# Kernel optimization log

Measured on AMD Instinct MI355X. Metric: run time of the kernel, lower is better.

The kernel has to match this reference:

```python
import jax, jax.numpy as jnp
import numpy as np

NTYPES = 2
B, N, MNEI = 4, 512, 100
M = MNEI * NTYPES          # neighbor slots = maxNeighborNum * ntypes
EMB_LAST = 100             # embedding net sizes [25, 50, 100]
FIT_H = 240
M2 = 16
RMIN, RMAX = 0.5, 6.0


def setup_inputs():
    key = jax.random.key(0)
    ks = jax.random.split(key, 24)
    r = jax.random.uniform(ks[0], (B, N, M), minval=0.6, maxval=7.0)
    v = jax.random.normal(ks[1], (B, N, M, 3))
    v = v / jnp.linalg.norm(v, axis=-1, keepdims=True)
    keep = jax.random.uniform(ks[2], (B, N, M)) < 0.7
    ImageDR = jnp.concatenate([r[..., None], r[..., None] * v], axis=-1)
    ImageDR = jnp.where(keep[..., None], ImageDR, 0.0).astype(jnp.float32)
    Imagetype_map = jax.random.randint(ks[3], (N,), 0, NTYPES)
    list_neigh = jax.random.randint(ks[4], (B, N, M), 0, N + 1)
    type_map = jnp.arange(NTYPES)
    davg = (0.01 * jax.random.normal(ks[5], (NTYPES, M, 4))).astype(jnp.float32)
    dstd = (1.0 + 0.1 * jax.random.uniform(ks[6], (NTYPES, M, 4))).astype(jnp.float32)

    def w(k, shape, fan):
        return (jax.random.normal(k, shape) / np.sqrt(fan)).astype(jnp.float32)

    def b(k, shape):
        return (0.1 * jax.random.normal(k, shape)).astype(jnp.float32)

    emb_W0 = w(ks[7], (NTYPES, NTYPES, 1, 25), 1)
    emb_b0 = b(ks[8], (NTYPES, NTYPES, 25))
    emb_W1 = w(ks[9], (NTYPES, NTYPES, 25, 50), 25)
    emb_b1 = b(ks[10], (NTYPES, NTYPES, 50))
    emb_W2 = w(ks[11], (NTYPES, NTYPES, 50, 100), 50)
    emb_b2 = b(ks[12], (NTYPES, NTYPES, 100))
    fin = M2 * EMB_LAST
    fit_W0 = w(ks[13], (NTYPES, fin, FIT_H), fin)
    fit_b0 = b(ks[14], (NTYPES, FIT_H))
    fit_W1 = w(ks[15], (NTYPES, FIT_H, FIT_H), FIT_H)
    fit_b1 = b(ks[16], (NTYPES, FIT_H))
    fit_W2 = w(ks[17], (NTYPES, FIT_H, FIT_H), FIT_H)
    fit_b2 = b(ks[18], (NTYPES, FIT_H))
    fit_W3 = w(ks[19], (NTYPES, FIT_H, 1), FIT_H)
    fit_b3 = b(ks[20], (NTYPES, 1))
    energy_shift = jnp.array([-3.37, -5.21], dtype=jnp.float32)
    return dict(list_neigh=list_neigh, Imagetype_map=Imagetype_map, type_map=type_map,
                ImageDR=ImageDR, nghost=0, davg=davg, dstd=dstd,
                emb_W0=emb_W0, emb_b0=emb_b0, emb_W1=emb_W1, emb_b1=emb_b1,
                emb_W2=emb_W2, emb_b2=emb_b2,
                fit_W0=fit_W0, fit_b0=fit_b0, fit_W1=fit_W1, fit_b1=fit_b1,
                fit_W2=fit_W2, fit_b2=fit_b2, fit_W3=fit_W3, fit_b3=fit_b3,
                energy_shift=energy_shift)


def _emb(s, W0, b0, W1, b1, W2, b2):
    # DeepPot-SE embedding net with doubling resnet connections
    h = jnp.tanh(s @ W0 + b0)                                   # [..., 25]
    h = jnp.tanh(h @ W1 + b1) + jnp.concatenate([h, h], -1)     # [..., 50]
    return jnp.tanh(h @ W2 + b2) + jnp.concatenate([h, h], -1)  # [..., 100]


def _fit(d, W0, b0, W1, b1, W2, b2, W3, b3):
    h = jnp.tanh(d @ W0 + b0)
    h = h + jnp.tanh(h @ W1 + b1)
    h = h + jnp.tanh(h @ W2 + b2)
    return h @ W3 + b3


def _forward(ImageDR, davg, dstd,
             emb_W0, emb_b0, emb_W1, emb_b1, emb_W2, emb_b2,
             fit_W0, fit_b0, fit_W1, fit_b1, fit_W2, fit_b2, fit_W3, fit_b3,
             energy_shift, Imagetype_map):
    Bsz, Nat, Mtot, _ = ImageDR.shape
    m = Mtot // NTYPES
    R = ImageDR[..., 0]
    Rsafe = jnp.where(R > 1e-5, R, 1.0)
    # smooth switching function s(r): 1/r below Rmin, polynomial taper to Rmax
    u = (R - RMIN) / (RMAX - RMIN)
    mid = (u ** 3 * (-6.0 * u * u + 15.0 * u - 10.0) + 1.0) / Rsafe
    S = jnp.where((R > 0) & (R < RMIN), 1.0 / Rsafe,
                  jnp.where((R > RMIN) & (R < RMAX), mid, 0.0))
    msk = (jnp.abs(R) > 1e-5)[..., None]
    Ri = jnp.concatenate([S[..., None],
                          jnp.where(msk, (S / Rsafe)[..., None] * ImageDR[..., 1:4], 0.0)],
                         axis=-1)                                    # [B,N,M,4] = (s, s*x/r, s*y/r, s*z/r)
    # per-center-type normalization (irregular gather of stats)
    Rn = (Ri - davg[Imagetype_map][None]) / dstd[Imagetype_map][None]
    tmask = [(Imagetype_map == i).astype(Rn.dtype)[None, :, None, None] for i in range(NTYPES)]
    xyz = jnp.zeros((Bsz, Nat, 4, EMB_LAST), Rn.dtype)
    for j in range(NTYPES):                                          # neighbor-type slice
        sl = Rn[:, :, j * m:(j + 1) * m, :]                          # [B,N,m,4]
        s = sl[..., 0:1]
        G = jnp.zeros(sl.shape[:3] + (EMB_LAST,), sl.dtype)
        for i in range(NTYPES):                                      # center type -> pair net (i, j)
            G = G + tmask[i] * _emb(s, emb_W0[i, j], emb_b0[i, j],
                                    emb_W1[i, j], emb_b1[i, j], emb_W2[i, j], emb_b2[i, j])
        xyz = xyz + jnp.einsum('bnmk,bnmc->bnkc', sl, G)
    xyz = xyz / (m * NTYPES)
    # descriptor D = (Ri^T G)^T (Ri^T G)[:, :M2], flattened -> [B,N,EMB_LAST*M2]
    D = jnp.einsum('bnkc,bnkd->bncd', xyz, xyz[..., :M2]).reshape(Bsz, Nat, -1)
    Ei = jnp.zeros((Bsz, Nat), D.dtype)
    for i in range(NTYPES):
        e = _fit(D, fit_W0[i], fit_b0[i], fit_W1[i], fit_b1[i],
                 fit_W2[i], fit_b2[i], fit_W3[i], fit_b3[i])[..., 0] + energy_shift[i]
        Ei = Ei + tmask[i][:, :, 0, 0] * e
    Etot = jnp.sum(Ei, axis=1)
    return Etot, Ei


def reference(list_neigh, Imagetype_map, type_map, ImageDR, nghost, davg, dstd,
              emb_W0, emb_b0, emb_W1, emb_b1, emb_W2, emb_b2,
              fit_W0, fit_b0, fit_W1, fit_b1, fit_W2, fit_b2, fit_W3, fit_b3,
              energy_shift):
    return _forward(ImageDR, davg, dstd,
                    emb_W0, emb_b0, emb_W1, emb_b1, emb_W2, emb_b2,
                    fit_W0, fit_b0, fit_W1, fit_b1, fit_W2, fit_b2, fit_W3, fit_b3,
                    energy_shift, Imagetype_map)
```

## Files before the change

kernel.cpp:

```cpp
#include <hip/hip_runtime.h>
#include <math.h>

#define NT 2
#define BSZ 4
#define NAT 512
#define NATOMS 2048
#define NNEI 200
#define EMB 100
#define FITH 240
#define DDIM 1600
#define TBK 1024

#define BIAS_F  16
#define W3C_F   (BIAS_F + 3 * 512)
#define USH_BYTE 8320
#define TBL_U   0
#define W0T_U   409600
#define W1T_U   (W0T_U + 819200)
#define W2T_U   (W1T_U + 262144)
#define D_U     (W2T_U + 262144)
#define H0_U    (D_U + 3276800)
#define H1_U    (H0_U + 1048576)
#define USH_END (H1_U + 1048576)
#define WS_NEED ((size_t)USH_BYTE + (size_t)USH_END * 2)

typedef short s8v __attribute__((ext_vector_type(8)));
typedef float f4v __attribute__((ext_vector_type(4)));

__device__ __forceinline__ float ftanh(float x) {
    float ax = fabsf(x);
    float e = __expf(2.0f * ax);
    float t = 1.0f - __fdividef(2.0f, e + 1.0f);
    return (x < 0.0f) ? -t : t;
}
__device__ __forceinline__ unsigned short f2bf(float f) {
    unsigned u = __float_as_uint(f);
    u += 0x7FFFu + ((u >> 16) & 1u);
    return (unsigned short)(u >> 16);
}
__device__ __forceinline__ float bf2f(unsigned short s) {
    return __uint_as_float(((unsigned)s) << 16);
}
__device__ __forceinline__ float calc_S(float R) {
    float Rsafe = (R > 1e-5f) ? R : 1.0f;
    float u = (R - 0.5f) * (1.0f / 5.5f);
    float uu = u * u;
    float mid = (u * uu * (-6.0f * uu + 15.0f * u - 10.0f) + 1.0f) / Rsafe;
    float S = 0.0f;
    if (R > 0.0f && R < 0.5f)      S = 1.0f / Rsafe;
    else if (R > 0.5f && R < 6.0f) S = mid;
    return S;
}

#define N_W0 819200
#define N_W1 262144
#define N_W2 262144
#define N_B  1536
#define N_W3 512
#define N_EI 2048
__global__ void wtrans_kernel(const float* __restrict__ fW0, const float* __restrict__ fW1,
                              const float* __restrict__ fW2,
                              const float* __restrict__ fb0, const float* __restrict__ fb1,
                              const float* __restrict__ fb2,
                              const float* __restrict__ fW3, const float* __restrict__ fb3,
                              const float* __restrict__ eshift, const int* __restrict__ itype,
                              float* __restrict__ ws, float* __restrict__ out) {
    unsigned short* u0 = (unsigned short*)((char*)ws + USH_BYTE);
    int id = blockIdx.x * 256 + threadIdx.x;
    if (id < N_W0) {
        int n = id / 1600, k = id - n * 1600;
        float v = 0.0f;
        if (n < 240)                  v = fW0[(size_t)k * 240 + n];
        else if (n >= 256 && n < 496) v = fW0[(size_t)(1600 + k) * 240 + (n - 256)];
        u0[W0T_U + id] = f2bf(v);
        return;
    }
    id -= N_W0;
    if (id < N_W1) {
        int n = id / 512, k = id - n * 512;
        float v = 0.0f;
        if (n < 240 && k < 240)       v = fW1[(size_t)k * 240 + n];
        else if (n >= 256 && n < 496 && k >= 256 && k < 496)
                                      v = fW1[(size_t)(240 + (k - 256)) * 240 + (n - 256)];
        u0[W1T_U + id] = f2bf(v);
        return;
    }
    id -= N_W1;
    if (id < N_W2) {
        int n = id / 512, k = id - n * 512;
        float v = 0.0f;
        if (n < 240 && k < 240)       v = fW2[(size_t)k * 240 + n];
        else if (n >= 256 && n < 496 && k >= 256 && k < 496)
                                      v = fW2[(size_t)(240 + (k - 256)) * 240 + (n - 256)];
        u0[W2T_U + id] = f2bf(v);
        return;
    }
    id -= N_W2;
    if (id < N_B) {
        int l = id / 512, n = id - l * 512;
        const float* fb = (l == 0) ? fb0 : (l == 1) ? fb1 : fb2;
        float v = 0.0f;
        if (n < 240)                  v = fb[n];
        else if (n >= 256 && n < 496) v = fb[240 + (n - 256)];
        ws[BIAS_F + l * 512 + n] = v;
        return;
    }
    id -= N_B;
    if (id < N_W3) {
        int n = id;
        float v = 0.0f;
        if (n < 240)                  v = fW3[n];
        else if (n >= 256 && n < 496) v = fW3[240 + (n - 256)];
        ws[W3C_F + n] = v;
        return;
    }
    id -= N_W3;
    if (id < N_EI) {
        int t = itype[id & (NAT - 1)];
        out[4 + id] = fb3[t] + eshift[t];
    }
}

__global__ void __launch_bounds__(256) table_kernel(
    const float* __restrict__ davg, const float* __restrict__ dstd,
    const float* __restrict__ eW0, const float* __restrict__ eb0,
    const float* __restrict__ eW1, const float* __restrict__ eb1,
    const float* __restrict__ eW2, const float* __restrict__ eb2,
    float* __restrict__ ws)
{
    __shared__ float los[100], his[100];
    __shared__ float rng[2];
    __shared__ float h0s[8][25];
    __shared__ float h1s[8][50];
    const int bx = blockIdx.x;
    const int nid = bx >> 7;
    const int kb  = (bx & 127) * 8;
    const int t = nid >> 1, j = nid & 1;
    const int tid = threadIdx.x;

    if (tid < 100) {
        int m = j * 100 + tid;
        float av = davg[(t * NNEI + m) * 4];
        float sd = dstd[(t * NNEI + m) * 4];
        float inv = __fdividef(1.0f, sd);
        float a = (0.0f - av) * inv;
        float b = (2.0f - av) * inv;
        los[tid] = fminf(a, b);
        his[tid] = fmaxf(a, b);
    }
    __syncthreads();
    if (tid == 0) {
        float lo = los[0], hi = his[0];
        for (int i = 1; i < 100; ++i) { lo = fminf(lo, los[i]); hi = fmaxf(hi, his[i]); }
        rng[0] = lo; rng[1] = hi - lo;
        if (kb == 0) {
            ws[nid * 2] = lo;
            ws[nid * 2 + 1] = (float)(TBK - 1) / (hi - lo);
        }
    }
    __syncthreads();
    const float smin = rng[0], span = rng[1];
    const float* W0 = eW0 + nid * 25;
    const float* B0 = eb0 + nid * 25;
    if (tid < 200) {
        int q = tid / 25, a = tid % 25;
        float s = smin + span * ((float)(kb + q) * (1.0f / (TBK - 1)));
        h0s[q][a] = ftanh(fmaf(s, W0[a], B0[a]));
    }
    __syncthreads();
    const float* W1 = eW1 + nid * 1250;
    const float* B1 = eb1 + nid * 50;
    for (int idx = tid; idx < 400; idx += 256) {
        int q = idx / 50, cc = idx % 50;
        float acc = B1[cc];
#pragma unroll
        for (int a = 0; a < 25; ++a) acc = fmaf(h0s[q][a], W1[a * 50 + cc], acc);
        h1s[q][cc] = ftanh(acc) + h0s[q][(cc < 25) ? cc : cc - 25];
    }
    __syncthreads();
    const float* W2 = eW2 + nid * 5000;
    const float* B2 = eb2 + nid * 100;
    unsigned short* tblu = (unsigned short*)((char*)ws + USH_BYTE) + TBL_U;
    for (int idx = tid; idx < 800; idx += 256) {
        int q = idx / 100, c = idx % 100;
        float acc = B2[c];
#pragma unroll
        for (int a = 0; a < 50; ++a) acc = fmaf(h1s[q][a], W2[a * 100 + c], acc);
        float g = ftanh(acc) + h1s[q][(c < 50) ? c : c - 50];
        tblu[(size_t)(nid * TBK + kb + q) * 100 + c] = f2bf(g);
    }
}

__global__ void __launch_bounds__(128) embed_kernel(
    const int* __restrict__ itype, const float* __restrict__ imagedr,
    const float* __restrict__ davg, const float* __restrict__ dstd,
    float* __restrict__ ws)
{
    __shared__ __align__(16) float4 srn[NNEI];
    __shared__ float sx[NNEI];
    __shared__ float part[2][400];
    const int atom = blockIdx.x;
    const int n = atom & (NAT - 1);
    const int tid = threadIdx.x;
    const int t = itype[n];
    unsigned short* u0 = (unsigned short*)((char*)ws + USH_BYTE);

    const float sm0 = ws[(t * 2 + 0) * 2], sc0 = ws[(t * 2 + 0) * 2 + 1];
    const float sm1 = ws[(t * 2 + 1) * 2], sc1 = ws[(t * 2 + 1) * 2 + 1];

    for (int m = tid; m < NNEI; m += 128) {
        float4 dr = ((const float4*)imagedr)[(size_t)atom * NNEI + m];
        float R = dr.x;
        float S = calc_S(R);
        float Rsafe = (R > 1e-5f) ? R : 1.0f;
        float sr = (fabsf(R) > 1e-5f) ? (S / Rsafe) : 0.0f;
        float4 av = ((const float4*)davg)[t * NNEI + m];
        float4 sd = ((const float4*)dstd)[t * NNEI + m];
        float4 rv;
        rv.x = (S         - av.x) / sd.x;
        rv.y = (sr * dr.y - av.y) / sd.y;
        rv.z = (sr * dr.z - av.z) / sd.z;
        rv.w = (sr * dr.w - av.w) / sd.w;
        srn[m] = rv;
        float smin = (m >= 100) ? sm1 : sm0;
        float scal = (m >= 100) ? sc1 : sc0;
        sx[m] = fminf(fmaxf((rv.x - smin) * scal, 0.0f), (float)(TBK - 2) + 0.9999f);
    }
    __syncthreads();

    const int w = tid >> 6, lane = tid & 63;
    const unsigned short* T = u0 + TBL_U + (size_t)(t * 2 + w) * TBK * EMB;
    const bool hi = (lane < 36);
    float xA0 = 0, xA1 = 0, xA2 = 0, xA3 = 0;
    float xB0 = 0, xB1 = 0, xB2 = 0, xB3 = 0;
#pragma unroll 2
    for (int mi = 0; mi < 100; ++mi) {
        int m = w * 100 + mi;
        float4 rv = srn[m];
        float x = sx[m];
        int i = (int)x;
        float f = x - (float)i;
        const unsigned short* Tr = T + (size_t)i * EMB;
        float g0 = bf2f(Tr[lane]);
        float g1 = bf2f(Tr[EMB + lane]);
        float g = fmaf(f, g1 - g0, g0);
        xA0 = fmaf(rv.x, g, xA0); xA1 = fmaf(rv.y, g, xA1);
        xA2 = fmaf(rv.z, g, xA2); xA3 = fmaf(rv.w, g, xA3);
        if (hi) {
            float h0v = bf2f(Tr[64 + lane]);
            float h1v = bf2f(Tr[EMB + 64 + lane]);
            float g2 = fmaf(f, h1v - h0v, h0v);
            xB0 = fmaf(rv.x, g2, xB0); xB1 = fmaf(rv.y, g2, xB1);
            xB2 = fmaf(rv.z, g2, xB2); xB3 = fmaf(rv.w, g2, xB3);
        }
    }
    part[w][0 * 100 + lane] = xA0; part[w][1 * 100 + lane] = xA1;
    part[w][2 * 100 + lane] = xA2; part[w][3 * 100 + lane] = xA3;
    if (hi) {
        part[w][0 * 100 + 64 + lane] = xB0; part[w][1 * 100 + 64 + lane] = xB1;
        part[w][2 * 100 + 64 + lane] = xB2; part[w][3 * 100 + 64 + lane] = xB3;
    }
    __syncthreads();
    const float inv = 1.0f / 200.0f;
    for (int idx = tid; idx < 400; idx += 128)
        part[0][idx] = (part[0][idx] + part[1][idx]) * inv;
    __syncthreads();
    unsigned short* Drow = u0 + D_U + (size_t)atom * DDIM;
    const float* xt = part[0];
    for (int idx = tid; idx < DDIM; idx += 128) {
        int c = idx >> 4, d = idx & 15;
        float s = xt[c] * xt[d] + xt[100 + c] * xt[100 + d]
                + xt[200 + c] * xt[200 + d] + xt[300 + c] * xt[300 + d];
        Drow[idx] = f2bf(s);
    }
}

__global__ void __launch_bounds__(64) gemm16_kernel(
    const unsigned short* __restrict__ A, int lda,
    const unsigned short* __restrict__ BT, int ldb,
    const float* __restrict__ bias,
    const unsigned short* __restrict__ Res,
    unsigned short* __restrict__ Out, int ldo,
    const float* __restrict__ w3c, const int* __restrict__ itype,
    float* __restrict__ out,
    int ksteps, int diag, int mode)
{
    const int lane = threadIdx.x;
    const int bx = blockIdx.x;
    const int by = blockIdx.y;
    const int m0 = by * 16, n0 = bx * 32;
    const int k0 = (diag && bx >= 8) ? 256 : 0;
    const int mr = lane & 15;
    const int q  = lane >> 4;
    const unsigned short* Ap  = A  + (size_t)(m0 + mr) * lda + k0 + q * 8;
    const unsigned short* B0p = BT + (size_t)(n0 + mr) * ldb + k0 + q * 8;
    const unsigned short* B1p = B0p + (size_t)16 * ldb;

    f4v acc0 = {0.0f, 0.0f, 0.0f, 0.0f};
    f4v acc1 = {0.0f, 0.0f, 0.0f, 0.0f};
#pragma unroll 2
    for (int kt = 0; kt < ksteps; ++kt) {
        s8v av = *(const s8v*)(Ap  + kt * 32);
        s8v b0 = *(const s8v*)(B0p + kt * 32);
        s8v b1 = *(const s8v*)(B1p + kt * 32);
        acc0 = __builtin_amdgcn_mfma_f32_16x16x32_bf16(av, b0, acc0, 0, 0, 0);
        acc1 = __builtin_amdgcn_mfma_f32_16x16x32_bf16(av, b1, acc1, 0, 0, 0);
    }

    const int g0 = n0 + mr, g1 = n0 + 16 + mr;
    const float bv0 = bias[g0], bv1 = bias[g1];
    if (mode < 2) {
#pragma unroll
        for (int r = 0; r < 4; ++r) {
            int row = m0 + q * 4 + r;
            size_t i0 = (size_t)row * ldo + g0;
            size_t i1 = (size_t)row * ldo + g1;
            float v0 = ftanh(acc0[r] + bv0);
            float v1 = ftanh(acc1[r] + bv1);
            if (mode == 1) { v0 += bf2f(Res[i0]); v1 += bf2f(Res[i1]); }
            Out[i0] = f2bf(v0); Out[i1] = f2bf(v1);
        }
    } else {
        const int seg = (bx >= 8);
        const float w30 = w3c[g0], w31 = w3c[g1];
#pragma unroll
        for (int r = 0; r < 4; ++r) {
            int row = m0 + q * 4 + r;
            size_t i0 = (size_t)row * ldo + g0;
            size_t i1 = (size_t)row * ldo + g1;
            float v0 = bf2f(Res[i0]) + ftanh(acc0[r] + bv0);
            float v1 = bf2f(Res[i1]) + ftanh(acc1[r] + bv1);
            float p = v0 * w30 + v1 * w31;
            p += __shfl_xor(p, 1, 16);
            p += __shfl_xor(p, 2, 16);
            p += __shfl_xor(p, 4, 16);
            p += __shfl_xor(p, 8, 16);
            if (mr == 0 && itype[row & (NAT - 1)] == seg)
                atomicAdd(&out[4 + row], p);
        }
    }
}

__global__ void etot_kernel(float* __restrict__ out) {
    const int b = blockIdx.x;
    float s = 0.0f;
    for (int n = threadIdx.x; n < NAT; n += 256) s += out[4 + b * NAT + n];
#pragma unroll
    for (int off = 32; off > 0; off >>= 1) s += __shfl_down(s, off, 64);
    __shared__ float rr[4];
    if ((threadIdx.x & 63) == 0) rr[threadIdx.x >> 6] = s;
    __syncthreads();
    if (threadIdx.x == 0) out[b] = rr[0] + rr[1] + rr[2] + rr[3];
}

__global__ void dp_atom_kernel(
    const int* __restrict__ itype, const float* __restrict__ imagedr,
    const float* __restrict__ davg, const float* __restrict__ dstd,
    const float* __restrict__ eW0, const float* __restrict__ eb0,
    const float* __restrict__ eW1, const float* __restrict__ eb1,
    const float* __restrict__ eW2, const float* __restrict__ eb2,
    const float* __restrict__ fW0, const float* __restrict__ fb0,
    const float* __restrict__ fW1, const float* __restrict__ fb1,
    const float* __restrict__ fW2, const float* __restrict__ fb2,
    const float* __restrict__ fW3, const float* __restrict__ fb3,
    const float* __restrict__ eshift, float* __restrict__ out)
{
    __shared__ __align__(16) float4 rn4[NNEI];
    __shared__ __align__(16) float  xyz[4 * EMB];
    __shared__ __align__(16) float  h0s[100 * 25];
    __shared__ __align__(16) float  smem[100 * 52];
    const int atom = blockIdx.x;
    const int n = atom & (NAT - 1);
    const int tid = threadIdx.x;
    const int t = itype[n];
    for (int m = tid; m < NNEI; m += 256) {
        float4 dr = ((const float4*)imagedr)[(size_t)atom * NNEI + m];
        float R = dr.x;
        float S = calc_S(R);
        float Rsafe = (R > 1e-5f) ? R : 1.0f;
        float sr = (fabsf(R) > 1e-5f) ? (S / Rsafe) : 0.0f;
        float4 av = ((const float4*)davg)[t * NNEI + m];
        float4 sd = ((const float4*)dstd)[t * NNEI + m];
        float4 rv;
        rv.x = (S - av.x) / sd.x; rv.y = (sr * dr.y - av.y) / sd.y;
        rv.z = (sr * dr.z - av.z) / sd.z; rv.w = (sr * dr.w - av.w) / sd.w;
        rn4[m] = rv;
    }
    const int c = tid & 127; const int mh = tid >> 7;
    float xp0 = 0, xp1 = 0, xp2 = 0, xp3 = 0;
    for (int j = 0; j < NT; ++j) {
        const int wb = t * NT + j;
        const float* W0 = eW0 + wb * 25; const float* B0 = eb0 + wb * 25;
        const float* W1 = eW1 + wb * 1250; const float* B1 = eb1 + wb * 50;
        const float* W2 = eW2 + wb * 5000; const float* B2 = eb2 + wb * 100;
        __syncthreads();
        for (int idx = tid; idx < 2500; idx += 256) {
            int m = idx / 25, a = idx - m * 25;
            h0s[idx] = ftanh(fmaf(rn4[j * 100 + m].x, W0[a], B0[a]));
        }
        __syncthreads();
        for (int idx = tid; idx < 5000; idx += 256) {
            int m = idx / 50, cc = idx - m * 50;
            const float* h0m = h0s + m * 25;
            float acc = B1[cc];
#pragma unroll
            for (int a = 0; a < 25; ++a) acc = fmaf(h0m[a], W1[a * 50 + cc], acc);
            smem[m * 52 + cc] = ftanh(acc) + h0m[(cc < 25) ? cc : cc - 25];
        }
        for (int idx = tid; idx < 200; idx += 256)
            smem[(idx >> 1) * 52 + 50 + (idx & 1)] = 0.0f;
        __syncthreads();
        if (c < EMB) {
            float w2c[52];
#pragma unroll
            for (int a = 0; a < 50; ++a) w2c[a] = W2[a * EMB + c];
            w2c[50] = 0; w2c[51] = 0;
            const float bc = B2[c];
            const int sk = (c < 50) ? c : c - 50;
            for (int i = 0; i < 50; ++i) {
                int m = mh * 50 + i;
                const float* h1m = smem + m * 52;
                float acc = bc;
#pragma unroll
                for (int q = 0; q < 13; ++q) {
                    float4 hv = ((const float4*)h1m)[q];
                    acc = fmaf(hv.x, w2c[4 * q], acc); acc = fmaf(hv.y, w2c[4 * q + 1], acc);
                    acc = fmaf(hv.z, w2c[4 * q + 2], acc); acc = fmaf(hv.w, w2c[4 * q + 3], acc);
                }
                float g = ftanh(acc) + h1m[sk];
                float4 rm = rn4[j * 100 + m];
                xp0 = fmaf(rm.x, g, xp0); xp1 = fmaf(rm.y, g, xp1);
                xp2 = fmaf(rm.z, g, xp2); xp3 = fmaf(rm.w, g, xp3);
            }
        }
    }
    __syncthreads();
    const float inv = 1.0f / 200.0f;
    if (mh == 0 && c < EMB) {
        xyz[c] = xp0 * inv; xyz[EMB + c] = xp1 * inv;
        xyz[2 * EMB + c] = xp2 * inv; xyz[3 * EMB + c] = xp3 * inv;
    }
    __syncthreads();
    if (mh == 1 && c < EMB) {
        xyz[c] += xp0 * inv; xyz[EMB + c] += xp1 * inv;
        xyz[2 * EMB + c] += xp2 * inv; xyz[3 * EMB + c] += xp3 * inv;
    }
    __syncthreads();
    float* Dld = smem;
    for (int idx = tid; idx < DDIM; idx += 256) {
        int cc = idx >> 4, d = idx & 15;
        Dld[idx] = xyz[cc] * xyz[d] + xyz[EMB + cc] * xyz[EMB + d]
                 + xyz[2 * EMB + cc] * xyz[2 * EMB + d] + xyz[3 * EMB + cc] * xyz[3 * EMB + d];
    }
    __syncthreads();
    float* hA = smem + DDIM; float* hB = hA + FITH; float* h2 = hB + FITH; float* red = h2 + FITH;
    if (tid < FITH) {
        const float* W = fW0 + (size_t)t * DDIM * FITH;
        float acc = fb0[t * FITH + tid];
        for (int f = 0; f < DDIM; f += 4) {
            float4 dv = *(const float4*)(Dld + f);
            acc = fmaf(dv.x, W[f * FITH + tid], acc); acc = fmaf(dv.y, W[(f + 1) * FITH + tid], acc);
            acc = fmaf(dv.z, W[(f + 2) * FITH + tid], acc); acc = fmaf(dv.w, W[(f + 3) * FITH + tid], acc);
        }
        hA[tid] = ftanh(acc);
    }
    __syncthreads();
    if (tid < FITH) {
        const float* W = fW1 + t * FITH * FITH;
        float acc = fb1[t * FITH + tid];
        for (int f = 0; f < FITH; f += 4) {
            float4 hv = *(const float4*)(hA + f);
            acc = fmaf(hv.x, W[f * FITH + tid], acc); acc = fmaf(hv.y, W[(f + 1) * FITH + tid], acc);
            acc = fmaf(hv.z, W[(f + 2) * FITH + tid], acc); acc = fmaf(hv.w, W[(f + 3) * FITH + tid], acc);
        }
        hB[tid] = hA[tid] + ftanh(acc);
    }
    __syncthreads();
    if (tid < FITH) {
        const float* W = fW2 + t * FITH * FITH;
        float acc = fb2[t * FITH + tid];
        for (int f = 0; f < FITH; f += 4) {
            float4 hv = *(const float4*)(hB + f);
            acc = fmaf(hv.x, W[f * FITH + tid], acc); acc = fmaf(hv.y, W[(f + 1) * FITH + tid], acc);
            acc = fmaf(hv.z, W[(f + 2) * FITH + tid], acc); acc = fmaf(hv.w, W[(f + 3) * FITH + tid], acc);
        }
        h2[tid] = hB[tid] + ftanh(acc);
    }
    __syncthreads();
    float p = (tid < FITH) ? h2[tid] * fW3[t * FITH + tid] : 0.0f;
#pragma unroll
    for (int off = 32; off > 0; off >>= 1) p += __shfl_down(p, off, 64);
    if ((tid & 63) == 0) red[tid >> 6] = p;
    __syncthreads();
    if (tid == 0) out[4 + atom] = red[0] + red[1] + red[2] + red[3] + fb3[t] + eshift[t];
}

extern "C" void kernel_launch(void* const* d_in, const int* in_sizes, int n_in,
                              void* d_out, int out_size, void* d_ws, size_t ws_size,
                              hipStream_t stream) {
    const int*   itype   = (const int*)  d_in[1];
    const float* imagedr = (const float*)d_in[3];
    const float* davg    = (const float*)d_in[5];
    const float* dstd    = (const float*)d_in[6];
    const float* eW0     = (const float*)d_in[7];
    const float* eb0     = (const float*)d_in[8];
    const float* eW1     = (const float*)d_in[9];
    const float* eb1     = (const float*)d_in[10];
    const float* eW2     = (const float*)d_in[11];
    const float* eb2     = (const float*)d_in[12];
    const float* fW0     = (const float*)d_in[13];
    const float* fb0     = (const float*)d_in[14];
    const float* fW1     = (const float*)d_in[15];
    const float* fb1     = (const float*)d_in[16];
    const float* fW2     = (const float*)d_in[17];
    const float* fb2     = (const float*)d_in[18];
    const float* fW3     = (const float*)d_in[19];
    const float* fb3     = (const float*)d_in[20];
    const float* eshift  = (const float*)d_in[21];
    float* out = (float*)d_out;
    float* ws  = (float*)d_ws;

    if (ws_size >= WS_NEED) {
        unsigned short* u0 = (unsigned short*)((char*)ws + USH_BYTE);
        const int n_ids = N_W0 + N_W1 + N_W2 + N_B + N_W3 + N_EI;
        wtrans_kernel<<<(n_ids + 255) / 256, 256, 0, stream>>>(
            fW0, fW1, fW2, fb0, fb1, fb2, fW3, fb3, eshift, itype, ws, out);
        table_kernel<<<512, 256, 0, stream>>>(davg, dstd, eW0, eb0, eW1, eb1, eW2, eb2, ws);
        embed_kernel<<<NATOMS, 128, 0, stream>>>(itype, imagedr, davg, dstd, ws);
        gemm16_kernel<<<dim3(16, 128), 64, 0, stream>>>(
            u0 + D_U, DDIM, u0 + W0T_U, DDIM, ws + BIAS_F,
            nullptr, u0 + H0_U, 512, nullptr, nullptr, nullptr, 50, 0, 0);
        gemm16_kernel<<<dim3(16, 128), 64, 0, stream>>>(
            u0 + H0_U, 512, u0 + W1T_U, 512, ws + BIAS_F + 512,
            u0 + H0_U, u0 + H1_U, 512, nullptr, nullptr, nullptr, 8, 1, 0 + 1);
        gemm16_kernel<<<dim3(16, 128), 64, 0, stream>>>(
            u0 + H1_U, 512, u0 + W2T_U, 512, ws + BIAS_F + 1024,
            u0 + H1_U, nullptr, 512, ws + W3C_F, itype, out, 8, 1, 2);
        etot_kernel<<<BSZ, 256, 0, stream>>>(out);
    } else {
        dp_atom_kernel<<<NATOMS, 256, 0, stream>>>(itype, imagedr, davg, dstd,
            eW0, eb0, eW1, eb1, eW2, eb2,
            fW0, fb0, fW1, fb1, fW2, fb2, fW3, fb3, eshift, out);
        etot_kernel<<<BSZ, 256, 0, stream>>>(out);
    }
}
```

Before: 202.9 us.

## Widen fitting GEMM tiles to 64 columns and split-K the first layer

Replaces the generic 16x32-tile GEMM with two specialized kernels that compute 16x64 output tiles, so each A fragment load feeds four MFMAs instead of two. The first fitting layer now uses two waves that each take half of the K=1600 range, with the partial sums combined through shared memory before the bias+tanh epilogue. The residual layers hardcode K=256 per segment and fully unroll. The embed loop unroll factor also goes from 2 to 4. These trade more registers per wave and fewer blocks for better operand reuse and more parallel depth on the long K loop.

```diff
diff --git a/kernel.cpp b/kernel.cpp
--- a/kernel.cpp
+++ b/kernel.cpp
@@ -233,7 +233,7 @@
     const bool hi = (lane < 36);
     float xA0 = 0, xA1 = 0, xA2 = 0, xA3 = 0;
     float xB0 = 0, xB1 = 0, xB2 = 0, xB3 = 0;
-#pragma unroll 2
+#pragma unroll 4
     for (int mi = 0; mi < 100; ++mi) {
         int m = w * 100 + mi;
         float4 rv = srn[m];
@@ -275,62 +275,113 @@
     }
 }
 
-__global__ void __launch_bounds__(64) gemm16_kernel(
-    const unsigned short* __restrict__ A, int lda,
-    const unsigned short* __restrict__ BT, int ldb,
+__global__ void __launch_bounds__(128) gemm0_kernel(
+    const unsigned short* __restrict__ A,
+    const unsigned short* __restrict__ BT,
     const float* __restrict__ bias,
-    const unsigned short* __restrict__ Res,
-    unsigned short* __restrict__ Out, int ldo,
+    unsigned short* __restrict__ Out)
+{
+    __shared__ float lred[64][17];
+    const int tid = threadIdx.x;
+    const int w = tid >> 6, lane = tid & 63;
+    const int mr = lane & 15, q = lane >> 4;
+    const int n0 = blockIdx.x * 64;
+    const int m0 = blockIdx.y * 16;
+    const unsigned short* Ap = A  + (size_t)(m0 + mr) * DDIM + w * 800 + q * 8;
+    const unsigned short* Bp = BT + (size_t)(n0 + mr) * DDIM + w * 800 + q * 8;
+
+    f4v a0 = {0,0,0,0}, a1 = {0,0,0,0}, a2 = {0,0,0,0}, a3 = {0,0,0,0};
+#pragma unroll 5
+    for (int kt = 0; kt < 25; ++kt) {
+        s8v av = *(const s8v*)(Ap + kt * 32);
+        s8v b0 = *(const s8v*)(Bp + kt * 32);
+        s8v b1 = *(const s8v*)(Bp + 16 * DDIM + kt * 32);
+        s8v b2 = *(const s8v*)(Bp + 32 * DDIM + kt * 32);
+        s8v b3 = *(const s8v*)(Bp + 48 * DDIM + kt * 32);
+        a0 = __builtin_amdgcn_mfma_f32_16x16x32_bf16(av, b0, a0, 0, 0, 0);
+        a1 = __builtin_amdgcn_mfma_f32_16x16x32_bf16(av, b1, a1, 0, 0, 0);
+        a2 = __builtin_amdgcn_mfma_f32_16x16x32_bf16(av, b2, a2, 0, 0, 0);
+        a3 = __builtin_amdgcn_mfma_f32_16x16x32_bf16(av, b3, a3, 0, 0, 0);
+    }
+    if (w == 1) {
+#pragma unroll
+        for (int r = 0; r < 4; ++r) {
+            lred[lane][r]      = a0[r];
+            lred[lane][4 + r]  = a1[r];
+            lred[lane][8 + r]  = a2[r];
+            lred[lane][12 + r] = a3[r];
+        }
+    }
+    __syncthreads();
+    if (w == 0) {
+#pragma unroll
+        for (int j = 0; j < 4; ++j) {
+            const int col = n0 + j * 16 + mr;
+            const float bv = bias[col];
+            f4v* ap = (j == 0) ? &a0 : (j == 1) ? &a1 : (j == 2) ? &a2 : &a3;
+#pragma unroll
+            for (int r = 0; r < 4; ++r) {
+                float s = (*ap)[r] + lred[lane][j * 4 + r] + bv;
+                int row = m0 + q * 4 + r;
+                Out[(size_t)row * 512 + col] = f2bf(ftanh(s));
+            }
+        }
+    }
+}
+
+__global__ void __launch_bounds__(64) gemmr_kernel(
+    const unsigned short* __restrict__ A, const unsigned short* __restrict__ BT,
+    const float* __restrict__ bias, const unsigned short* __restrict__ Res,
+    unsigned short* __restrict__ Out,
     const float* __restrict__ w3c, const int* __restrict__ itype,
-    float* __restrict__ out,
-    int ksteps, int diag, int mode)
+    float* __restrict__ out, int mode)
 {
     const int lane = threadIdx.x;
+    const int mr = lane & 15, q = lane >> 4;
     const int bx = blockIdx.x;
-    const int by = blockIdx.y;
-    const int m0 = by * 16, n0 = bx * 32;
-    const int k0 = (diag && bx >= 8) ? 256 : 0;
-    const int mr = lane & 15;
-    const int q  = lane >> 4;
-    const unsigned short* Ap  = A  + (size_t)(m0 + mr) * lda + k0 + q * 8;
-    const unsigned short* B0p = BT + (size_t)(n0 + mr) * ldb + k0 + q * 8;
-    const unsigned short* B1p = B0p + (size_t)16 * ldb;
-
-    f4v acc0 = {0.0f, 0.0f, 0.0f, 0.0f};
-    f4v acc1 = {0.0f, 0.0f, 0.0f, 0.0f};
-#pragma unroll 2
-    for (int kt = 0; kt < ksteps; ++kt) {
-        s8v av = *(const s8v*)(Ap  + kt * 32);
-        s8v b0 = *(const s8v*)(B0p + kt * 32);
-        s8v b1 = *(const s8v*)(B1p + kt * 32);
-        acc0 = __builtin_amdgcn_mfma_f32_16x16x32_bf16(av, b0, acc0, 0, 0, 0);
-        acc1 = __builtin_amdgcn_mfma_f32_16x16x32_bf16(av, b1, acc1, 0, 0, 0);
-    }
-
-    const int g0 = n0 + mr, g1 = n0 + 16 + mr;
-    const float bv0 = bias[g0], bv1 = bias[g1];
-    if (mode < 2) {
+    const int n0 = bx * 64;
+    const int m0 = blockIdx.y * 16;
+    const int k0 = (bx >= 4) ? 256 : 0;
+    const unsigned short* Ap = A  + (size_t)(m0 + mr) * 512 + k0 + q * 8;
+    const unsigned short* Bp = BT + (size_t)(n0 + mr) * 512 + k0 + q * 8;
+
+    f4v a0 = {0,0,0,0}, a1 = {0,0,0,0}, a2 = {0,0,0,0}, a3 = {0,0,0,0};
+#pragma unroll
+    for (int kt = 0; kt < 8; ++kt) {
+        s8v av = *(const s8v*)(Ap + kt * 32);
+        s8v b0 = *(const s8v*)(Bp + kt * 32);
+        s8v b1 = *(const s8v*)(Bp + 16 * 512 + kt * 32);
+        s8v b2 = *(const s8v*)(Bp + 32 * 512 + kt * 32);
+        s8v b3 = *(const s8v*)(Bp + 48 * 512 + kt * 32);
+        a0 = __builtin_amdgcn_mfma_f32_16x16x32_bf16(av, b0, a0, 0, 0, 0);
+        a1 = __builtin_amdgcn_mfma_f32_16x16x32_bf16(av, b1, a1, 0, 0, 0);
+        a2 = __builtin_amdgcn_mfma_f32_16x16x32_bf16(av, b2, a2, 0, 0, 0);
+        a3 = __builtin_amdgcn_mfma_f32_16x16x32_bf16(av, b3, a3, 0, 0, 0);
+    }
+    const float bv0 = bias[n0 + mr],      bv1 = bias[n0 + 16 + mr];
+    const float bv2 = bias[n0 + 32 + mr], bv3 = bias[n0 + 48 + mr];
+    if (mode == 1) {
 #pragma unroll
         for (int r = 0; r < 4; ++r) {
             int row = m0 + q * 4 + r;
-            size_t i0 = (size_t)row * ldo + g0;
-            size_t i1 = (size_t)row * ldo + g1;
-            float v0 = ftanh(acc0[r] + bv0);
-            float v1 = ftanh(acc1[r] + bv1);
-            if (mode == 1) { v0 += bf2f(Res[i0]); v1 += bf2f(Res[i1]); }
-            Out[i0] = f2bf(v0); Out[i1] = f2bf(v1);
+            size_t base = (size_t)row * 512 + n0 + mr;
+            Out[base]      = f2bf(bf2f(Res[base])      + ftanh(a0[r] + bv0));
+            Out[base + 16] = f2bf(bf2f(Res[base + 16]) + ftanh(a1[r] + bv1));
+            Out[base + 32] = f2bf(bf2f(Res[base + 32]) + ftanh(a2[r] + bv2));
+            Out[base + 48] = f2bf(bf2f(Res[base + 48]) + ftanh(a3[r] + bv3));
         }
     } else {
-        const int seg = (bx >= 8);
-        const float w30 = w3c[g0], w31 = w3c[g1];
+        const int seg = (bx >= 4);
+        const float w30 = w3c[n0 + mr],      w31 = w3c[n0 + 16 + mr];
+        const float w32 = w3c[n0 + 32 + mr], w33 = w3c[n0 + 48 + mr];
 #pragma unroll
         for (int r = 0; r < 4; ++r) {
             int row = m0 + q * 4 + r;
-            size_t i0 = (size_t)row * ldo + g0;
-            size_t i1 = (size_t)row * ldo + g1;
-            float v0 = bf2f(Res[i0]) + ftanh(acc0[r] + bv0);
-            float v1 = bf2f(Res[i1]) + ftanh(acc1[r] + bv1);
-            float p = v0 * w30 + v1 * w31;
+            size_t base = (size_t)row * 512 + n0 + mr;
+            float p = (bf2f(Res[base])      + ftanh(a0[r] + bv0)) * w30
+                    + (bf2f(Res[base + 16]) + ftanh(a1[r] + bv1)) * w31
+                    + (bf2f(Res[base + 32]) + ftanh(a2[r] + bv2)) * w32
+                    + (bf2f(Res[base + 48]) + ftanh(a3[r] + bv3)) * w33;
             p += __shfl_xor(p, 1, 16);
             p += __shfl_xor(p, 2, 16);
             p += __shfl_xor(p, 4, 16);
@@ -527,15 +578,14 @@
             fW0, fW1, fW2, fb0, fb1, fb2, fW3, fb3, eshift, itype, ws, out);
         table_kernel<<<512, 256, 0, stream>>>(davg, dstd, eW0, eb0, eW1, eb1, eW2, eb2, ws);
         embed_kernel<<<NATOMS, 128, 0, stream>>>(itype, imagedr, davg, dstd, ws);
-        gemm16_kernel<<<dim3(16, 128), 64, 0, stream>>>(
-            u0 + D_U, DDIM, u0 + W0T_U, DDIM, ws + BIAS_F,
-            nullptr, u0 + H0_U, 512, nullptr, nullptr, nullptr, 50, 0, 0);
-        gemm16_kernel<<<dim3(16, 128), 64, 0, stream>>>(
-            u0 + H0_U, 512, u0 + W1T_U, 512, ws + BIAS_F + 512,
-            u0 + H0_U, u0 + H1_U, 512, nullptr, nullptr, nullptr, 8, 1, 0 + 1);
-        gemm16_kernel<<<dim3(16, 128), 64, 0, stream>>>(
-            u0 + H1_U, 512, u0 + W2T_U, 512, ws + BIAS_F + 1024,
-            u0 + H1_U, nullptr, 512, ws + W3C_F, itype, out, 8, 1, 2);
+        gemm0_kernel<<<dim3(8, 128), 128, 0, stream>>>(
+            u0 + D_U, u0 + W0T_U, ws + BIAS_F, u0 + H0_U);
+        gemmr_kernel<<<dim3(8, 128), 64, 0, stream>>>(
+            u0 + H0_U, u0 + W1T_U, ws + BIAS_F + 512, u0 + H0_U, u0 + H1_U,
+            nullptr, nullptr, nullptr, 1);
+        gemmr_kernel<<<dim3(8, 128), 64, 0, stream>>>(
+            u0 + H1_U, u0 + W2T_U, ws + BIAS_F + 1024, u0 + H1_U, nullptr,
+            ws + W3C_F, itype, out, 2);
         etot_kernel<<<BSZ, 256, 0, stream>>>(out);
     } else {
         dp_atom_kernel<<<NATOMS, 256, 0, stream>>>(itype, imagedr, davg, dstd,
```

Result: faster. 192.3 us (-5.2%).
